# Kernel optimization log

Measured on AMD Instinct MI355X. Metric: run time of the kernel, lower is better.

Reference implementation:

```python
import jax, jax.numpy as jnp
import numpy as np

B, C, H, W = 2, 256, 32, 32
D_MODEL = C
D_INNER = 2 * D_MODEL          # 512
D_STATE = 16
DT_RANK = (D_MODEL + 15) // 16  # 16
D_CONV = 4
LN_EPS = 1e-5


def setup_inputs() -> dict:
    key = jax.random.key(0)
    ks = jax.random.split(key, 32)

    def nrm(k, shape, s=0.02):
        return (jax.random.normal(k, shape) * s).astype(jnp.float32)

    inp = {"x": jax.random.normal(ks[0], (B, C, H, W), dtype=jnp.float32)}
    # LayerNorm params
    inp["ln1_w"] = jnp.ones((D_MODEL,), jnp.float32)
    inp["ln1_b"] = jnp.zeros((D_MODEL,), jnp.float32)
    inp["ln2_w"] = jnp.ones((D_MODEL,), jnp.float32)
    inp["ln2_b"] = jnp.zeros((D_MODEL,), jnp.float32)
    # Two MambaBlocks with identical structure
    for i, p in enumerate(["m1", "m2"]):
        o = 1 + i * 11
        inp[p + "_in_w"] = nrm(ks[o + 0], (D_MODEL, 2 * D_INNER))
        inp[p + "_in_b"] = jnp.zeros((2 * D_INNER,), jnp.float32)
        inp[p + "_conv_w"] = nrm(ks[o + 1], (D_INNER, 1, D_CONV), 0.1)
        inp[p + "_conv_b"] = jnp.zeros((D_INNER,), jnp.float32)
        inp[p + "_xproj_w"] = nrm(ks[o + 2], (D_INNER, DT_RANK + 2 * D_STATE))
        inp[p + "_dt_w"] = nrm(ks[o + 3], (DT_RANK, D_INNER), 0.1)
        inp[p + "_dt_b"] = (jax.random.uniform(ks[o + 4], (D_INNER,)) * 0.1 - 4.0).astype(jnp.float32)
        # S4D-real init: A[d, n] = n+1
        inp[p + "_A_log"] = jnp.log(jnp.broadcast_to(jnp.arange(1, D_STATE + 1, dtype=jnp.float32), (D_INNER, D_STATE)))
        inp[p + "_D"] = jnp.ones((D_INNER,), jnp.float32)
        inp[p + "_out_w"] = nrm(ks[o + 5], (D_INNER, D_MODEL))
        inp[p + "_out_b"] = jnp.zeros((D_MODEL,), jnp.float32)
    return inp


def layernorm(x, w, b):
    mu = jnp.mean(x, axis=-1, keepdims=True)
    var = jnp.mean(jnp.square(x - mu), axis=-1, keepdims=True)
    return (x - mu) * jax.lax.rsqrt(var + LN_EPS) * w + b


def mamba_block(x, in_w, in_b, conv_w, conv_b, xproj_w, dt_w, dt_b, A_log, Dp, out_w, out_b):
    # x: (b, h, w, c) -> flatten spatial dims into the scan sequence
    b, h, w, c = x.shape
    L = h * w
    u = x.reshape(b, L, c)
    xr = u @ in_w + in_b                       # (b, L, 2*d_inner)
    xs, res = jnp.split(xr, 2, axis=-1)
    # depthwise causal conv1d over L
    xc = jnp.transpose(xs, (0, 2, 1))          # (b, d_inner, L)
    xc = jax.lax.conv_general_dilated(
        xc, conv_w, (1,), [(D_CONV - 1, 0)],
        dimension_numbers=("NCH", "OIH", "NCH"),
        feature_group_count=D_INNER) + conv_b[None, :, None]
    xs = jax.nn.silu(jnp.transpose(xc, (0, 2, 1)))  # (b, L, d_inner)
    # input-dependent SSM params
    x_dbl = xs @ xproj_w                       # (b, L, dt_rank + 2*n)
    dt, Bm, Cm = jnp.split(x_dbl, [DT_RANK, DT_RANK + D_STATE], axis=-1)
    delta = jax.nn.softplus(dt @ dt_w + dt_b)  # (b, L, d_inner)
    A = -jnp.exp(A_log)                        # (d_inner, n)
    dA = jnp.exp(delta[..., None] * A)                         # (b, L, d, n)
    dBu = delta[..., None] * Bm[:, :, None, :] * xs[..., None]  # (b, L, d, n)

    def step(hst, ins):
        dA_t, dBu_t, C_t = ins
        hst = dA_t * hst + dBu_t               # (b, d, n)
        y_t = jnp.einsum("bdn,bn->bd", hst, C_t)
        return hst, y_t

    h0 = jnp.zeros((b, D_INNER, D_STATE), dtype=xs.dtype)
    _, ys = jax.lax.scan(step, h0,
                         (jnp.swapaxes(dA, 0, 1), jnp.swapaxes(dBu, 0, 1), jnp.swapaxes(Cm, 0, 1)))
    y = jnp.swapaxes(ys, 0, 1) + xs * Dp       # (b, L, d_inner)
    y = y * jax.nn.silu(res)
    out = y @ out_w + out_b                    # (b, L, c)
    return out.reshape(b, h, w, c)


def reference(x, ln1_w, ln1_b, ln2_w, ln2_b,
              m1_in_w, m1_in_b, m1_conv_w, m1_conv_b, m1_xproj_w, m1_dt_w, m1_dt_b, m1_A_log, m1_D, m1_out_w, m1_out_b,
              m2_in_w, m2_in_b, m2_conv_w, m2_conv_b, m2_xproj_w, m2_dt_w, m2_dt_b, m2_A_log, m2_D, m2_out_w, m2_out_b):
    xt = jnp.transpose(x, (0, 2, 3, 1))  # b c h w -> b h w c
    xt = xt + layernorm(mamba_block(xt, m1_in_w, m1_in_b, m1_conv_w, m1_conv_b, m1_xproj_w,
                                    m1_dt_w, m1_dt_b, m1_A_log, m1_D, m1_out_w, m1_out_b), ln1_w, ln1_b)
    xt = jnp.flip(xt, axis=3)  # flip channel axis, as in the original
    xt = xt + layernorm(mamba_block(xt, m2_in_w, m2_in_b, m2_conv_w, m2_conv_b, m2_xproj_w,
                                    m2_dt_w, m2_dt_b, m2_A_log, m2_D, m2_out_w, m2_out_b), ln2_w, ln2_b)
    xt = jnp.flip(xt, axis=3)
    return jnp.transpose(xt, (0, 3, 1, 2))  # b h w c -> b c h w
```

## Files before the change

### kernel.cpp

```cpp
#include <hip/hip_runtime.h>
#include <hip/hip_bf16.h>
#include <math.h>

#define L 1024
#define NB 2
#define DM 256
#define DI 512
#define DS 16
#define NC 64
#define CL 16

typedef unsigned int u32;
typedef unsigned short u16;
typedef short s16x8 __attribute__((ext_vector_type(8)));
typedef float f32x4 __attribute__((ext_vector_type(4)));

__device__ __forceinline__ float sigmoidf_(float x){ return 1.f/(1.f+__expf(-x)); }
__device__ __forceinline__ u16 f2bf(float v){
  u32 x = __float_as_uint(v);
  return (u16)((x + 0x7fffu + ((x >> 16) & 1u)) >> 16);
}
__device__ __forceinline__ float bf2f(u16 v){ return __uint_as_float((u32)v << 16); }

__device__ __forceinline__ void gload_lds16(const void* g, void* l){
  __builtin_amdgcn_global_load_lds((const __attribute__((address_space(1))) u32*)g,
                                   (__attribute__((address_space(3))) u32*)l, 16, 0, 0);
}

__device__ __forceinline__ void wave_reduce2(float& a, float& b){
  #pragma unroll
  for (int m=32; m; m>>=1){ a += __shfl_xor(a, m, 64); b += __shfl_xor(b, m, 64); }
}

#define SEG1 262144
#define SEG2 294912
#define SEG3 131072
#define SEGP (SEG1+SEG2+SEG3)
__global__ __launch_bounds__(256) void k_prep_trans(const float* __restrict__ x,
    float* __restrict__ u, u16* __restrict__ ub,
    const float* __restrict__ inw1, const float* __restrict__ xpw1, const float* __restrict__ dtw1, const float* __restrict__ outw1,
    const float* __restrict__ inw2, const float* __restrict__ xpw2, const float* __restrict__ dtw2, const float* __restrict__ outw2,
    u16* __restrict__ Wt1i, u16* __restrict__ Wt1x, u16* __restrict__ Wt1o,
    u16* __restrict__ Wt2i, u16* __restrict__ Wt2x, u16* __restrict__ Wt2o){
  __shared__ float T[64][65];
  if (blockIdx.x < 128){
    int t = threadIdx.x;
    int bidx = blockIdx.x;
    int lt = bidx & 15, ct = (bidx >> 4) & 3, b = bidx >> 6;
    int l0 = lt*64, c0 = ct*64;
    int lsub = (t & 15)*4, csub = t >> 4;
    #pragma unroll
    for (int i=0;i<4;++i){
      int c = csub + i*16;
      float4 v = *(const float4*)(x + ((size_t)(b*256 + c0 + c))*1024 + l0 + lsub);
      T[lsub+0][c]=v.x; T[lsub+1][c]=v.y; T[lsub+2][c]=v.z; T[lsub+3][c]=v.w;
    }
    __syncthreads();
    int cw = (t & 15)*4, lw = t >> 4;
    #pragma unroll
    for (int i=0;i<4;++i){
      int l = lw + i*16;
      float4 v = make_float4(T[l][cw], T[l][cw+1], T[l][cw+2], T[l][cw+3]);
      size_t o = ((size_t)(b*1024 + l0 + l))*256 + c0 + cw;
      *(float4*)(u + o) = v;
      *(ushort4*)(ub + o) = make_ushort4(f2bf(v.x), f2bf(v.y), f2bf(v.z), f2bf(v.w));
    }
    return;
  }
  int g = (blockIdx.x - 128)*256 + threadIdx.x;
  int p = g >= SEGP;
  int r = g - p*SEGP;
  const float* inw = p ? inw2 : inw1;  const float* xpw = p ? xpw2 : xpw1;
  const float* dtw = p ? dtw2 : dtw1;  const float* outw = p ? outw2 : outw1;
  u16* Wti = p ? Wt2i : Wt1i; u16* Wtx = p ? Wt2x : Wt1x;
  u16* Wto = p ? Wt2o : Wt1o;
  if (r < SEG1){
    int n = r >> 8, k = r & 255;
    Wti[r] = f2bf(inw[(size_t)k*1024 + n]);
  } else if (r < SEG1+SEG2){
    int q = r - SEG1; int n = q >> 9, k = q & 511;
    float v;
    if (n < 512){
      float acc = 0.f;
      #pragma unroll
      for (int j=0;j<16;++j) acc = fmaf(xpw[k*48 + j], dtw[j*512 + n], acc);
      v = acc;
    } else if (n < 544){
      v = xpw[k*48 + 16 + (n - 512)];
    } else v = 0.f;
    Wtx[q] = f2bf(v);
  } else {
    int q = r - SEG1 - SEG2; int n = q >> 9, k = q & 511;
    Wto[q] = f2bf(outw[(size_t)k*256 + n]);
  }
}

__global__ __launch_bounds__(256) void k_gemm_mfma(const u16* __restrict__ A,
    const u16* __restrict__ Wt, const float* __restrict__ bias,
    float* __restrict__ C, int M, int N, int K){
  __shared__ __align__(16) u16 As[64*64];
  __shared__ __align__(16) u16 Bs[64*64];
  int tid = threadIdx.x, lane = tid & 63, wid = tid >> 6;
  int bm = blockIdx.y * 64, bn = blockIdx.x * 64;
  int wm = (wid >> 1) * 32, wn = (wid & 1) * 32;
  int lrow = lane & 15, lg = lane >> 4;
  int srow = tid >> 3, ssl = tid & 7;
  int sswz = ssl ^ (srow & 7);
  f32x4 acc[2][2] = {};
  for (int k0 = 0; k0 < K; k0 += 64){
    #pragma unroll
    for (int i = 0; i < 2; ++i){
      int row = srow + i*32;
      gload_lds16(A  + (size_t)(bm + row)*K + k0 + sswz*8, &As[row*64 + ssl*8]);
      gload_lds16(Wt + (size_t)(bn + row)*K + k0 + sswz*8, &Bs[row*64 + ssl*8]);
    }
    __syncthreads();
    #pragma unroll
    for (int ks = 0; ks < 2; ++ks){
      int kg = ks*4 + lg;
      int swz = (kg ^ (lrow & 7)) << 3;
      s16x8 a[2], b[2];
      #pragma unroll
      for (int f = 0; f < 2; ++f){
        a[f] = *(const s16x8*)&As[(wm + f*16 + lrow)*64 + swz];
        b[f] = *(const s16x8*)&Bs[(wn + f*16 + lrow)*64 + swz];
      }
      #pragma unroll
      for (int i = 0; i < 2; ++i)
        #pragma unroll
        for (int j = 0; j < 2; ++j)
          acc[i][j] = __builtin_amdgcn_mfma_f32_16x16x32_bf16(a[i], b[j], acc[i][j], 0, 0, 0);
    }
    __syncthreads();
  }
  #pragma unroll
  for (int j = 0; j < 2; ++j){
    int col = bn + wn + j*16 + lrow;
    if (col < N){
      float bv = bias ? bias[col] : 0.f;
      #pragma unroll
      for (int i = 0; i < 2; ++i)
        #pragma unroll
        for (int r = 0; r < 4; ++r){
          int row = bm + wm + i*16 + lg*4 + r;
          C[(size_t)row*N + col] = acc[i][j][r] + bv;
        }
    }
  }
}

__global__ __launch_bounds__(256) void k_conv_t(const float* __restrict__ xr,
    const float* __restrict__ cw, const float* __restrict__ cb,
    u16* __restrict__ xscT, u16* __restrict__ xscbl, u16* __restrict__ sresT){
  __shared__ float T[67*68];
  int tid = threadIdx.x;
  int d0 = (blockIdx.x & 7) * 64;
  int bm = (blockIdx.x >> 3) * 64;
  bool bstart = (bm & 1023) == 0;
  for (int base = tid; base < 67*16; base += 256){
    int r = base >> 4, q = base & 15;
    float4 v;
    if (r < 3 && bstart) v = make_float4(0.f,0.f,0.f,0.f);
    else v = *(const float4*)(xr + (size_t)(bm - 3 + r)*1024 + d0 + q*4);
    *(float4*)&T[r*68 + q*4] = v;
  }
  __syncthreads();
  int d_local = tid >> 2, lseg = tid & 3;
  int d = d0 + d_local;
  float4 wv = *(const float4*)(cw + d*4);
  float cbv = cb[d];
  float fo[16];
  float xm3 = T[(lseg*16+0)*68 + d_local];
  float xm2 = T[(lseg*16+1)*68 + d_local];
  float xm1 = T[(lseg*16+2)*68 + d_local];
  #pragma unroll
  for (int i=0;i<16;++i){
    float xc = T[(lseg*16+i+3)*68 + d_local];
    float o = cbv;
    o = fmaf(wv.x, xm3, o); o = fmaf(wv.y, xm2, o);
    o = fmaf(wv.z, xm1, o); o = fmaf(wv.w, xc, o);
    o *= sigmoidf_(o);
    fo[i] = o;
    xm3 = xm2; xm2 = xm1; xm1 = xc;
  }
  {
    s16x8 v0, v1;
    #pragma unroll
    for (int i=0;i<8;++i){ v0[i] = (short)f2bf(fo[i]); v1[i] = (short)f2bf(fo[8+i]); }
    u16* dst = xscT + (size_t)d*2048 + bm + lseg*16;
    *(s16x8*)dst = v0; *(s16x8*)(dst+8) = v1;
  }
  __syncthreads();
  #pragma unroll
  for (int i=0;i<16;++i) T[(lseg*16+i+3)*68 + d_local] = fo[i];
  __syncthreads();
  {
    int l_local = tid >> 2, dseg = tid & 3;
    s16x8 p0, p1;
    #pragma unroll
    for (int i=0;i<8;++i){
      p0[i] = (short)f2bf(T[(l_local+3)*68 + dseg*16 + i]);
      p1[i] = (short)f2bf(T[(l_local+3)*68 + dseg*16 + 8 + i]);
    }
    u16* dst2 = xscbl + (size_t)(bm + l_local)*512 + d0 + dseg*16;
    *(s16x8*)dst2 = p0; *(s16x8*)(dst2+8) = p1;
  }
  __syncthreads();
  for (int base = tid; base < 64*16; base += 256){
    int r = base >> 4, q = base & 15;
    float4 v = *(const float4*)(xr + (size_t)(bm + r)*1024 + 512 + d0 + q*4);
    v.x *= sigmoidf_(v.x); v.y *= sigmoidf_(v.y);
    v.z *= sigmoidf_(v.z); v.w *= sigmoidf_(v.w);
    *(float4*)&T[r*68 + q*4] = v;
  }
  __syncthreads();
  {
    s16x8 r0, r1;
    #pragma unroll
    for (int i=0;i<8;++i){
      r0[i] = (short)f2bf(T[(lseg*16+i)*68 + d_local]);
      r1[i] = (short)f2bf(T[(lseg*16+8+i)*68 + d_local]);
    }
    u16* dst3 = sresT + (size_t)d*2048 + bm + lseg*16;
    *(s16x8*)dst3 = r0; *(s16x8*)(dst3+8) = r1;
  }
}

__global__ __launch_bounds__(256) void k_xproj(const u16* __restrict__ A,
    const u16* __restrict__ Wt, const float* __restrict__ dtb,
    u16* __restrict__ dltT, u16* __restrict__ BCb){
  __shared__ __align__(16) float smem[64*69];
  u16* As = (u16*)smem;
  u16* Bs = As + 4096;
  int tid = threadIdx.x, lane = tid & 63, wid = tid >> 6;
  int bn = blockIdx.x, bm = blockIdx.y * 64;
  int bn64 = bn * 64;
  int wm = (wid >> 1) * 32, wn = (wid & 1) * 32;
  int lrow = lane & 15, lg = lane >> 4;
  int srow = tid >> 3, ssl = tid & 7;
  int sswz = ssl ^ (srow & 7);
  f32x4 acc[2][2] = {};
  for (int k0 = 0; k0 < 512; k0 += 64){
    #pragma unroll
    for (int i = 0; i < 2; ++i){
      int row = srow + i*32;
      gload_lds16(A  + (size_t)(bm + row)*512 + k0 + sswz*8, &As[row*64 + ssl*8]);
      gload_lds16(Wt + (size_t)(bn64 + row)*512 + k0 + sswz*8, &Bs[row*64 + ssl*8]);
    }
    __syncthreads();
    #pragma unroll
    for (int ks = 0; ks < 2; ++ks){
      int kg = ks*4 + lg;
      int swz = (kg ^ (lrow & 7)) << 3;
      s16x8 a[2], b[2];
      #pragma unroll
      for (int f = 0; f < 2; ++f){
        a[f] = *(const s16x8*)&As[(wm + f*16 + lrow)*64 + swz];
        b[f] = *(const s16x8*)&Bs[(wn + f*16 + lrow)*64 + swz];
      }
      #pragma unroll
      for (int i = 0; i < 2; ++i)
        #pragma unroll
        for (int j = 0; j < 2; ++j)
          acc[i][j] = __builtin_amdgcn_mfma_f32_16x16x32_bf16(a[i], b[j], acc[i][j], 0, 0, 0);
    }
    __syncthreads();
  }
  if (bn < 8){
    float* DT = smem;
    #pragma unroll
    for (int j=0;j<2;++j){
      int col_l = wn + j*16 + lrow;
      float bv = dtb[bn64 + col_l];
      #pragma unroll
      for (int i=0;i<2;++i)
        #pragma unroll
        for (int r=0;r<4;++r){
          int row_l = wm + i*16 + lg*4 + r;
          float a = acc[i][j][r] + bv;
          DT[row_l*69 + col_l] = fmaxf(a, 0.f) + log1pf(__expf(-fabsf(a)));
        }
    }
    __syncthreads();
    int c_local = tid >> 2, lseg = tid & 3;
    int dcol = bn64 + c_local;
    s16x8 v0, v1;
    #pragma unroll
    for (int i=0;i<8;++i){
      v0[i] = (short)f2bf(DT[(lseg*16+i)*69 + c_local]);
      v1[i] = (short)f2bf(DT[(lseg*16+8+i)*69 + c_local]);
    }
    u16* dst = dltT + (size_t)dcol*2048 + bm + lseg*16;
    *(s16x8*)dst = v0; *(s16x8*)(dst+8) = v1;
  } else {
    #pragma unroll
    for (int j=0;j<2;++j){
      int col_g = bn64 + wn + j*16 + lrow;
      if (col_g < 544){
        #pragma unroll
        for (int i=0;i<2;++i)
          #pragma unroll
          for (int r=0;r<4;++r){
            int row = bm + wm + i*16 + lg*4 + r;
            BCb[(size_t)row*32 + (col_g - 512)] = f2bf(acc[i][j][r]);
          }
      }
    }
  }
}

__global__ __launch_bounds__(256) void k_scan(const u16* __restrict__ dltT,
    const u16* __restrict__ xscT, const u16* __restrict__ BCb,
    const u16* __restrict__ sresT, const float* __restrict__ A_log,
    const float* __restrict__ Dp, u16* __restrict__ ygb){
  __shared__ float hbuf[64][68];
  __shared__ float SsumL[64][4];
  int tid = threadIdx.x;
  int chunk = tid >> 2, dl = tid & 3;
  int b = blockIdx.x >> 7, d0 = (blockIdx.x & 127) << 2;
  int d = d0 + dl;
  float A[DS];
  #pragma unroll
  for (int n=0;n<DS;++n) A[n] = -__expf(A_log[d*DS + n]);
  size_t cbase = (size_t)d*2048 + b*1024 + chunk*16;
  s16x8 dv0 = *(const s16x8*)(dltT + cbase);
  s16x8 dv1 = *(const s16x8*)(dltT + cbase + 8);
  s16x8 xv0 = *(const s16x8*)(xscT + cbase);
  s16x8 xv1 = *(const s16x8*)(xscT + cbase + 8);
  float dr[16], xq[16];
  #pragma unroll
  for (int i=0;i<8;++i){
    dr[i] = bf2f((u16)dv0[i]); dr[8+i] = bf2f((u16)dv1[i]);
    xq[i] = bf2f((u16)xv0[i]); xq[8+i] = bf2f((u16)xv1[i]);
  }
  float h[DS];
  #pragma unroll
  for (int n=0;n<DS;++n) h[n] = 0.f;
  float S = 0.f;
  int rbase = b*1024 + chunk*16;
  #pragma unroll
  for (int t=0;t<16;++t){
    const u16* bp = BCb + (size_t)(rbase + t)*32;
    s16x8 b0 = *(const s16x8*)bp;
    s16x8 b1 = *(const s16x8*)(bp + 8);
    float dlt = dr[t]; S += dlt;
    float dx = dlt * xq[t];
    #pragma unroll
    for (int n=0;n<8;++n) h[n] = fmaf(__expf(dlt*A[n]), h[n], dx*bf2f((u16)b0[n]));
    #pragma unroll
    for (int n=0;n<8;++n) h[8+n] = fmaf(__expf(dlt*A[8+n]), h[8+n], dx*bf2f((u16)b1[n]));
  }
  #pragma unroll
  for (int n=0;n<DS;++n) hbuf[chunk][dl*16+n] = h[n];
  SsumL[chunk][dl] = S;
  __syncthreads();
  if (tid < 64){
    int dl2 = tid & 3, n2 = tid >> 2;
    float An = -__expf(A_log[(d0+dl2)*DS + n2]);
    float hh = 0.f;
    for (int c=0;c<NC;++c){
      float he  = hbuf[c][dl2*16+n2];
      float dec = __expf(An * SsumL[c][dl2]);
      float nh  = fmaf(dec, hh, he);
      hbuf[c][dl2*16+n2] = hh;
      hh = nh;
    }
  }
  __syncthreads();
  #pragma unroll
  for (int n=0;n<DS;++n) h[n] = hbuf[chunk][dl*16+n];
  s16x8 s0 = *(const s16x8*)(sresT + cbase);
  s16x8 s1 = *(const s16x8*)(sresT + cbase + 8);
  float sr[16];
  #pragma unroll
  for (int i=0;i<8;++i){ sr[i] = bf2f((u16)s0[i]); sr[8+i] = bf2f((u16)s1[i]); }
  float Dv = Dp[d];
  #pragma unroll
  for (int t=0;t<16;++t){
    const u16* bp = BCb + (size_t)(rbase + t)*32;
    s16x8 b0 = *(const s16x8*)bp;
    s16x8 b1 = *(const s16x8*)(bp + 8);
    s16x8 c0 = *(const s16x8*)(bp + 16);
    s16x8 c1 = *(const s16x8*)(bp + 24);
    float dlt = dr[t];
    float dx = dlt * xq[t];
    float y = 0.f;
    #pragma unroll
    for (int n=0;n<8;++n){
      h[n] = fmaf(__expf(dlt*A[n]), h[n], dx*bf2f((u16)b0[n]));
      y = fmaf(h[n], bf2f((u16)c0[n]), y);
    }
    #pragma unroll
    for (int n=0;n<8;++n){
      h[8+n] = fmaf(__expf(dlt*A[8+n]), h[8+n], dx*bf2f((u16)b1[n]));
      y = fmaf(h[8+n], bf2f((u16)c1[n]), y);
    }
    y = fmaf(xq[t], Dv, y);
    ygb[(size_t)(rbase + t)*512 + d] = f2bf(y * sr[t]);
  }
}

__global__ __launch_bounds__(256) void k_ln_flip(const float* __restrict__ mo, const float* __restrict__ resid,
    const float* __restrict__ w, const float* __restrict__ bias,
    float* __restrict__ u2, u16* __restrict__ u2b){
  int row = blockIdx.x*4 + (threadIdx.x >> 6);
  int lane = threadIdx.x & 63;
  int c4 = lane*4;
  float4 xv = *(const float4*)(mo + (size_t)row*256 + c4);
  float s1 = xv.x+xv.y+xv.z+xv.w;
  float s2 = xv.x*xv.x+xv.y*xv.y+xv.z*xv.z+xv.w*xv.w;
  wave_reduce2(s1, s2);
  float mu = s1*(1.f/256), var = s2*(1.f/256) - mu*mu;
  float inv = rsqrtf(var + 1e-5f);
  float4 rv = *(const float4*)(resid + (size_t)row*256 + c4);
  float4 wv = *(const float4*)(w + c4);
  float4 bv = *(const float4*)(bias + c4);
  float o0 = rv.x + (xv.x-mu)*inv*wv.x + bv.x;
  float o1 = rv.y + (xv.y-mu)*inv*wv.y + bv.y;
  float o2 = rv.z + (xv.z-mu)*inv*wv.z + bv.z;
  float o3 = rv.w + (xv.w-mu)*inv*wv.w + bv.w;
  size_t o = (size_t)row*256 + (252 - c4);
  *(float4*)(u2 + o) = make_float4(o3, o2, o1, o0);
  *(ushort4*)(u2b + o) = make_ushort4(f2bf(o3), f2bf(o2), f2bf(o1), f2bf(o0));
}

__global__ __launch_bounds__(256) void k_ln_out(const float* __restrict__ mo, const float* __restrict__ resid,
    const float* __restrict__ w, const float* __restrict__ bias, float* __restrict__ out){
  int row = blockIdx.x*4 + (threadIdx.x >> 6);
  int lane = threadIdx.x & 63;
  int c4 = lane*4;
  int b = row >> 10, l = row & 1023;
  float4 xv = *(const float4*)(mo + (size_t)row*256 + c4);
  float s1 = xv.x+xv.y+xv.z+xv.w;
  float s2 = xv.x*xv.x+xv.y*xv.y+xv.z*xv.z+xv.w*xv.w;
  wave_reduce2(s1, s2);
  float mu = s1*(1.f/256), var = s2*(1.f/256) - mu*mu;
  float inv = rsqrtf(var + 1e-5f);
  float4 rv = *(const float4*)(resid + (size_t)row*256 + c4);
  float4 wv = *(const float4*)(w + c4);
  float4 bv = *(const float4*)(bias + c4);
  float o0 = rv.x + (xv.x-mu)*inv*wv.x + bv.x;
  float o1 = rv.y + (xv.y-mu)*inv*wv.y + bv.y;
  float o2 = rv.z + (xv.z-mu)*inv*wv.z + bv.z;
  float o3 = rv.w + (xv.w-mu)*inv*wv.w + bv.w;
  size_t base = ((size_t)b*256 + 255) << 10;
  out[base - ((size_t)(c4+0) << 10) + l] = o0;
  out[base - ((size_t)(c4+1) << 10) + l] = o1;
  out[base - ((size_t)(c4+2) << 10) + l] = o2;
  out[base - ((size_t)(c4+3) << 10) + l] = o3;
}

extern "C" void kernel_launch(void* const* d_in, const int* in_sizes, int n_in,
                              void* d_out, int out_size, void* d_ws, size_t ws_size,
                              hipStream_t stream) {
  const float* x    = (const float*)d_in[0];
  const float* ln1w = (const float*)d_in[1];
  const float* ln1b = (const float*)d_in[2];
  const float* ln2w = (const float*)d_in[3];
  const float* ln2b = (const float*)d_in[4];

  const float* m1[11]; const float* m2[11];
  for (int i=0;i<11;++i){ m1[i] = (const float*)d_in[5+i]; m2[i] = (const float*)d_in[16+i]; }

  float* ws = (float*)d_ws;
  float* u0    = ws;
  u16*   u0b   = (u16*)(ws + 524288);
  float* xr    = ws + 655360;
  u16*   xscbl = (u16*)(ws + 2752512);
  u16*   xscT  = (u16*)(ws + 3276800);
  u16*   sresT = (u16*)(ws + 3801088);
  u16*   dltT  = (u16*)(ws + 4325376);
  u16*   BCb   = (u16*)(ws + 4849664);
  u16*   ygb   = (u16*)(ws + 4882432);
  float* mo    = ws + 5406720;
  float* u2    = ws + 5931008;
  u16*   u2b   = (u16*)(ws + 6455296);
  u16*   Wt1i  = (u16*)(ws + 6586368);
  u16*   Wt1x  = (u16*)(ws + 6717440);
  u16*   Wt1o  = (u16*)(ws + 6864896);
  u16*   Wt2i  = (u16*)(ws + 6930432);
  u16*   Wt2x  = (u16*)(ws + 7061504);
  u16*   Wt2o  = (u16*)(ws + 7208960);

  dim3 b256(256);
  k_prep_trans<<<128 + 2*SEGP/256, b256, 0, stream>>>(x, u0, u0b,
      m1[0], m1[4], m1[5], m1[9], m2[0], m2[4], m2[5], m2[9],
      Wt1i, Wt1x, Wt1o, Wt2i, Wt2x, Wt2o);

  k_gemm_mfma<<<dim3(16,32), b256, 0, stream>>>(u0b, Wt1i, m1[1], xr, NB*L, 2*DI, DM);
  k_conv_t<<<256, b256, 0, stream>>>(xr, m1[2], m1[3], xscT, xscbl, sresT);
  k_xproj<<<dim3(9,32), b256, 0, stream>>>(xscbl, Wt1x, m1[6], dltT, BCb);
  k_scan<<<256, b256, 0, stream>>>(dltT, xscT, BCb, sresT, m1[7], m1[8], ygb);
  k_gemm_mfma<<<dim3(4,32), b256, 0, stream>>>(ygb, Wt1o, m1[10], mo, NB*L, DM, DI);
  k_ln_flip<<<512, b256, 0, stream>>>(mo, u0, ln1w, ln1b, u2, u2b);

  k_gemm_mfma<<<dim3(16,32), b256, 0, stream>>>(u2b, Wt2i, m2[1], xr, NB*L, 2*DI, DM);
  k_conv_t<<<256, b256, 0, stream>>>(xr, m2[2], m2[3], xscT, xscbl, sresT);
  k_xproj<<<dim3(9,32), b256, 0, stream>>>(xscbl, Wt2x, m2[6], dltT, BCb);
  k_scan<<<256, b256, 0, stream>>>(dltT, xscT, BCb, sresT, m2[7], m2[8], ygb);
  k_gemm_mfma<<<dim3(4,32), b256, 0, stream>>>(ygb, Wt2o, m2[10], mo, NB*L, DM, DI);
  k_ln_out<<<512, b256, 0, stream>>>(mo, u2, ln2w, ln2b, (float*)d_out);
}
```

Measured before the change: 128.1 us.

## Fuse in-proj epilogue with silu/transpose and out-proj with layernorm

The in-projection GEMM now writes the xs half directly as bf16 and applies silu plus a transpose to the residual half in its epilogue. This removes the fp32 xr intermediate and the residual pass that lived in the conv kernel. The out-projection GEMM is fused with layernorm, the residual add and the flip/transpose writes by having each block own full 256-column rows, which eliminates the mo buffer and two LN kernels. The trade-off is that the out-proj launch drops to only 32 blocks, so GPU occupancy is low, and xs is now rounded to bf16 before the conv.

Measured after the change: 138.0 us. 7.8% more time.

```diff
diff --git a/kernel.cpp b/kernel.cpp
--- a/kernel.cpp
+++ b/kernel.cpp
@@ -25,11 +25,6 @@
 __device__ __forceinline__ void gload_lds16(const void* g, void* l){
   __builtin_amdgcn_global_load_lds((const __attribute__((address_space(1))) u32*)g,
                                    (__attribute__((address_space(3))) u32*)l, 16, 0, 0);
-}
-
-__device__ __forceinline__ void wave_reduce2(float& a, float& b){
-  #pragma unroll
-  for (int m=32; m; m>>=1){ a += __shfl_xor(a, m, 64); b += __shfl_xor(b, m, 64); }
 }
 
 #define SEG1 262144
@@ -95,24 +90,26 @@
   }
 }
 
-__global__ __launch_bounds__(256) void k_gemm_mfma(const u16* __restrict__ A,
+__global__ __launch_bounds__(256) void k_in_proj(const u16* __restrict__ A,
     const u16* __restrict__ Wt, const float* __restrict__ bias,
-    float* __restrict__ C, int M, int N, int K){
-  __shared__ __align__(16) u16 As[64*64];
-  __shared__ __align__(16) u16 Bs[64*64];
+    u16* __restrict__ xsb, u16* __restrict__ sresT){
+  __shared__ __align__(16) float smem[64*65];
+  u16* As = (u16*)smem;
+  u16* Bs = As + 4096;
   int tid = threadIdx.x, lane = tid & 63, wid = tid >> 6;
-  int bm = blockIdx.y * 64, bn = blockIdx.x * 64;
+  int bn = blockIdx.x, bm = blockIdx.y * 64;
+  int bn64 = bn * 64;
   int wm = (wid >> 1) * 32, wn = (wid & 1) * 32;
   int lrow = lane & 15, lg = lane >> 4;
   int srow = tid >> 3, ssl = tid & 7;
   int sswz = ssl ^ (srow & 7);
   f32x4 acc[2][2] = {};
-  for (int k0 = 0; k0 < K; k0 += 64){
+  for (int k0 = 0; k0 < 256; k0 += 64){
     #pragma unroll
     for (int i = 0; i < 2; ++i){
       int row = srow + i*32;
-      gload_lds16(A  + (size_t)(bm + row)*K + k0 + sswz*8, &As[row*64 + ssl*8]);
-      gload_lds16(Wt + (size_t)(bn + row)*K + k0 + sswz*8, &Bs[row*64 + ssl*8]);
+      gload_lds16(A  + (size_t)(bm + row)*256 + k0 + sswz*8, &As[row*64 + ssl*8]);
+      gload_lds16(Wt + (size_t)(bn64 + row)*256 + k0 + sswz*8, &Bs[row*64 + ssl*8]);
     }
     __syncthreads();
     #pragma unroll
@@ -133,36 +130,68 @@
     }
     __syncthreads();
   }
-  #pragma unroll
-  for (int j = 0; j < 2; ++j){
-    int col = bn + wn + j*16 + lrow;
-    if (col < N){
-      float bv = bias ? bias[col] : 0.f;
-      #pragma unroll
-      for (int i = 0; i < 2; ++i)
-        #pragma unroll
-        for (int r = 0; r < 4; ++r){
-          int row = bm + wm + i*16 + lg*4 + r;
-          C[(size_t)row*N + col] = acc[i][j][r] + bv;
+  if (bn < 8){
+    #pragma unroll
+    for (int j=0;j<2;++j){
+      int col_l = wn + j*16 + lrow;
+      float bv = bias[bn64 + col_l];
+      #pragma unroll
+      for (int i=0;i<2;++i)
+        #pragma unroll
+        for (int r=0;r<4;++r){
+          int row_l = wm + i*16 + lg*4 + r;
+          xsb[(size_t)(bm + row_l)*512 + bn64 + col_l] = f2bf(acc[i][j][r] + bv);
         }
     }
-  }
-}
-
-__global__ __launch_bounds__(256) void k_conv_t(const float* __restrict__ xr,
+  } else {
+    float* CT = smem;
+    #pragma unroll
+    for (int j=0;j<2;++j){
+      int col_l = wn + j*16 + lrow;
+      float bv = bias[bn64 + col_l];
+      #pragma unroll
+      for (int i=0;i<2;++i)
+        #pragma unroll
+        for (int r=0;r<4;++r){
+          int row_l = wm + i*16 + lg*4 + r;
+          float o = acc[i][j][r] + bv;
+          CT[row_l*65 + col_l] = o * sigmoidf_(o);
+        }
+    }
+    __syncthreads();
+    int d_local = tid >> 2, lseg = tid & 3;
+    s16x8 r0, r1;
+    #pragma unroll
+    for (int i=0;i<8;++i){
+      r0[i] = (short)f2bf(CT[(lseg*16+i)*65 + d_local]);
+      r1[i] = (short)f2bf(CT[(lseg*16+8+i)*65 + d_local]);
+    }
+    u16* dst = sresT + (size_t)(bn64 - 512 + d_local)*2048 + bm + lseg*16;
+    *(s16x8*)dst = r0; *(s16x8*)(dst+8) = r1;
+  }
+}
+
+__global__ __launch_bounds__(256) void k_conv_t(const u16* __restrict__ xsb,
     const float* __restrict__ cw, const float* __restrict__ cb,
-    u16* __restrict__ xscT, u16* __restrict__ xscbl, u16* __restrict__ sresT){
+    u16* __restrict__ xscT, u16* __restrict__ xscbl){
   __shared__ float T[67*68];
   int tid = threadIdx.x;
   int d0 = (blockIdx.x & 7) * 64;
   int bm = (blockIdx.x >> 3) * 64;
   bool bstart = (bm & 1023) == 0;
-  for (int base = tid; base < 67*16; base += 256){
-    int r = base >> 4, q = base & 15;
-    float4 v;
-    if (r < 3 && bstart) v = make_float4(0.f,0.f,0.f,0.f);
-    else v = *(const float4*)(xr + (size_t)(bm - 3 + r)*1024 + d0 + q*4);
-    *(float4*)&T[r*68 + q*4] = v;
+  for (int base = tid; base < 67*8; base += 256){
+    int r = base >> 3, q = base & 7;
+    float v[8];
+    if (r < 3 && bstart){
+      #pragma unroll
+      for (int k=0;k<8;++k) v[k] = 0.f;
+    } else {
+      s16x8 hv = *(const s16x8*)(xsb + (size_t)(bm - 3 + r)*512 + d0 + q*8);
+      #pragma unroll
+      for (int k=0;k<8;++k) v[k] = bf2f((u16)hv[k]);
+    }
+    #pragma unroll
+    for (int k=0;k<8;++k) T[r*68 + q*8 + k] = v[k];
   }
   __syncthreads();
   int d_local = tid >> 2, lseg = tid & 3;
@@ -204,25 +233,6 @@
     }
     u16* dst2 = xscbl + (size_t)(bm + l_local)*512 + d0 + dseg*16;
     *(s16x8*)dst2 = p0; *(s16x8*)(dst2+8) = p1;
-  }
-  __syncthreads();
-  for (int base = tid; base < 64*16; base += 256){
-    int r = base >> 4, q = base & 15;
-    float4 v = *(const float4*)(xr + (size_t)(bm + r)*1024 + 512 + d0 + q*4);
-    v.x *= sigmoidf_(v.x); v.y *= sigmoidf_(v.y);
-    v.z *= sigmoidf_(v.z); v.w *= sigmoidf_(v.w);
-    *(float4*)&T[r*68 + q*4] = v;
-  }
-  __syncthreads();
-  {
-    s16x8 r0, r1;
-    #pragma unroll
-    for (int i=0;i<8;++i){
-      r0[i] = (short)f2bf(T[(lseg*16+i)*68 + d_local]);
-      r1[i] = (short)f2bf(T[(lseg*16+8+i)*68 + d_local]);
-    }
-    u16* dst3 = sresT + (size_t)d*2048 + bm + lseg*16;
-    *(s16x8*)dst3 = r0; *(s16x8*)(dst3+8) = r1;
   }
 }
 
@@ -400,54 +410,93 @@
   }
 }
 
-__global__ __launch_bounds__(256) void k_ln_flip(const float* __restrict__ mo, const float* __restrict__ resid,
-    const float* __restrict__ w, const float* __restrict__ bias,
-    float* __restrict__ u2, u16* __restrict__ u2b){
-  int row = blockIdx.x*4 + (threadIdx.x >> 6);
-  int lane = threadIdx.x & 63;
-  int c4 = lane*4;
-  float4 xv = *(const float4*)(mo + (size_t)row*256 + c4);
-  float s1 = xv.x+xv.y+xv.z+xv.w;
-  float s2 = xv.x*xv.x+xv.y*xv.y+xv.z*xv.z+xv.w*xv.w;
-  wave_reduce2(s1, s2);
-  float mu = s1*(1.f/256), var = s2*(1.f/256) - mu*mu;
-  float inv = rsqrtf(var + 1e-5f);
-  float4 rv = *(const float4*)(resid + (size_t)row*256 + c4);
-  float4 wv = *(const float4*)(w + c4);
-  float4 bv = *(const float4*)(bias + c4);
-  float o0 = rv.x + (xv.x-mu)*inv*wv.x + bv.x;
-  float o1 = rv.y + (xv.y-mu)*inv*wv.y + bv.y;
-  float o2 = rv.z + (xv.z-mu)*inv*wv.z + bv.z;
-  float o3 = rv.w + (xv.w-mu)*inv*wv.w + bv.w;
-  size_t o = (size_t)row*256 + (252 - c4);
-  *(float4*)(u2 + o) = make_float4(o3, o2, o1, o0);
-  *(ushort4*)(u2b + o) = make_ushort4(f2bf(o3), f2bf(o2), f2bf(o1), f2bf(o0));
-}
-
-__global__ __launch_bounds__(256) void k_ln_out(const float* __restrict__ mo, const float* __restrict__ resid,
-    const float* __restrict__ w, const float* __restrict__ bias, float* __restrict__ out){
-  int row = blockIdx.x*4 + (threadIdx.x >> 6);
-  int lane = threadIdx.x & 63;
-  int c4 = lane*4;
-  int b = row >> 10, l = row & 1023;
-  float4 xv = *(const float4*)(mo + (size_t)row*256 + c4);
-  float s1 = xv.x+xv.y+xv.z+xv.w;
-  float s2 = xv.x*xv.x+xv.y*xv.y+xv.z*xv.z+xv.w*xv.w;
-  wave_reduce2(s1, s2);
-  float mu = s1*(1.f/256), var = s2*(1.f/256) - mu*mu;
-  float inv = rsqrtf(var + 1e-5f);
-  float4 rv = *(const float4*)(resid + (size_t)row*256 + c4);
-  float4 wv = *(const float4*)(w + c4);
-  float4 bv = *(const float4*)(bias + c4);
-  float o0 = rv.x + (xv.x-mu)*inv*wv.x + bv.x;
-  float o1 = rv.y + (xv.y-mu)*inv*wv.y + bv.y;
-  float o2 = rv.z + (xv.z-mu)*inv*wv.z + bv.z;
-  float o3 = rv.w + (xv.w-mu)*inv*wv.w + bv.w;
-  size_t base = ((size_t)b*256 + 255) << 10;
-  out[base - ((size_t)(c4+0) << 10) + l] = o0;
-  out[base - ((size_t)(c4+1) << 10) + l] = o1;
-  out[base - ((size_t)(c4+2) << 10) + l] = o2;
-  out[base - ((size_t)(c4+3) << 10) + l] = o3;
+template<int MODE>
+__global__ __launch_bounds__(256) void k_gemm_out_ln(const u16* __restrict__ A,
+    const u16* __restrict__ Wt, const float* __restrict__ ob,
+    const float* __restrict__ resid, const float* __restrict__ lnw, const float* __restrict__ lnb,
+    float* __restrict__ out, u16* __restrict__ outb){
+  __shared__ __align__(16) u16 As[64*64];
+  __shared__ __align__(16) u16 Bs[256*64];
+  __shared__ float redS[2][64], redQ[2][64];
+  int tid = threadIdx.x, lane = tid & 63, wid = tid >> 6;
+  int bm = blockIdx.x * 64;
+  int wm = (wid & 1)*32, wn = (wid >> 1)*128;
+  int lrow = lane & 15, lg = lane >> 4;
+  int srow = tid >> 3, ssl = tid & 7;
+  int sswz = ssl ^ (srow & 7);
+  f32x4 acc[2][8] = {};
+  for (int k0=0;k0<512;k0+=64){
+    #pragma unroll
+    for (int i=0;i<2;++i){
+      int row = srow + i*32;
+      gload_lds16(A + (size_t)(bm+row)*512 + k0 + sswz*8, &As[row*64 + ssl*8]);
+    }
+    #pragma unroll
+    for (int i=0;i<8;++i){
+      int row = srow + i*32;
+      gload_lds16(Wt + (size_t)row*512 + k0 + sswz*8, &Bs[row*64 + ssl*8]);
+    }
+    __syncthreads();
+    #pragma unroll
+    for (int ks=0;ks<2;++ks){
+      int kg = ks*4 + lg;
+      int swz = (kg ^ (lrow & 7)) << 3;
+      s16x8 a[2], bq[8];
+      #pragma unroll
+      for (int f=0;f<2;++f) a[f] = *(const s16x8*)&As[(wm + f*16 + lrow)*64 + swz];
+      #pragma unroll
+      for (int j=0;j<8;++j) bq[j] = *(const s16x8*)&Bs[(wn + j*16 + lrow)*64 + swz];
+      #pragma unroll
+      for (int f=0;f<2;++f)
+        #pragma unroll
+        for (int j=0;j<8;++j)
+          acc[f][j] = __builtin_amdgcn_mfma_f32_16x16x32_bf16(a[f], bq[j], acc[f][j], 0, 0, 0);
+    }
+    __syncthreads();
+  }
+  float bv[8], lw[8], lb[8];
+  #pragma unroll
+  for (int j=0;j<8;++j){
+    int col = wn + j*16 + lrow;
+    bv[j] = ob[col]; lw[j] = lnw[col]; lb[j] = lnb[col];
+  }
+  #pragma unroll
+  for (int i=0;i<2;++i)
+    #pragma unroll
+    for (int r=0;r<4;++r){
+      float s=0.f, q=0.f;
+      #pragma unroll
+      for (int j=0;j<8;++j){ float v = acc[i][j][r] + bv[j]; s += v; q = fmaf(v, v, q); }
+      #pragma unroll
+      for (int m=1;m<=8;m<<=1){ s += __shfl_xor(s, m, 64); q += __shfl_xor(q, m, 64); }
+      if (lrow == 0){ int row = wm + i*16 + lg*4 + r; redS[wn>>7][row] = s; redQ[wn>>7][row] = q; }
+    }
+  __syncthreads();
+  #pragma unroll
+  for (int i=0;i<2;++i)
+    #pragma unroll
+    for (int r=0;r<4;++r){
+      int row = wm + i*16 + lg*4 + r;
+      int grow = bm + row;
+      float S = redS[0][row] + redS[1][row];
+      float Q = redQ[0][row] + redQ[1][row];
+      float mu = S * (1.f/256.f);
+      float var = Q * (1.f/256.f) - mu*mu;
+      float inv = rsqrtf(var + 1e-5f);
+      #pragma unroll
+      for (int j=0;j<8;++j){
+        int col = wn + j*16 + lrow;
+        float v = acc[i][j][r] + bv[j];
+        float o = resid[(size_t)grow*256 + col] + (v - mu)*inv*lw[j] + lb[j];
+        if (MODE == 0){
+          out[(size_t)grow*256 + 255 - col]  = o;
+          outb[(size_t)grow*256 + 255 - col] = f2bf(o);
+        } else {
+          int bb = grow >> 10, ll = grow & 1023;
+          out[(((size_t)bb*256) + (255 - col))*1024 + ll] = o;
+        }
+      }
+    }
 }
 
 extern "C" void kernel_launch(void* const* d_in, const int* in_sizes, int n_in,
@@ -465,39 +514,36 @@
   float* ws = (float*)d_ws;
   float* u0    = ws;
   u16*   u0b   = (u16*)(ws + 524288);
-  float* xr    = ws + 655360;
-  u16*   xscbl = (u16*)(ws + 2752512);
-  u16*   xscT  = (u16*)(ws + 3276800);
-  u16*   sresT = (u16*)(ws + 3801088);
-  u16*   dltT  = (u16*)(ws + 4325376);
-  u16*   BCb   = (u16*)(ws + 4849664);
-  u16*   ygb   = (u16*)(ws + 4882432);
-  float* mo    = ws + 5406720;
-  float* u2    = ws + 5931008;
-  u16*   u2b   = (u16*)(ws + 6455296);
-  u16*   Wt1i  = (u16*)(ws + 6586368);
-  u16*   Wt1x  = (u16*)(ws + 6717440);
-  u16*   Wt1o  = (u16*)(ws + 6864896);
-  u16*   Wt2i  = (u16*)(ws + 6930432);
-  u16*   Wt2x  = (u16*)(ws + 7061504);
-  u16*   Wt2o  = (u16*)(ws + 7208960);
+  u16*   xsb   = (u16*)(ws + 655360);
+  u16*   xscbl = (u16*)(ws + 1179648);
+  u16*   xscT  = (u16*)(ws + 1703936);
+  u16*   sresT = (u16*)(ws + 2228224);
+  u16*   dltT  = (u16*)(ws + 2752512);
+  u16*   BCb   = (u16*)(ws + 3276800);
+  u16*   ygb   = (u16*)(ws + 3309568);
+  float* u2    = ws + 3833856;
+  u16*   u2b   = (u16*)(ws + 4358144);
+  u16*   Wt1i  = (u16*)(ws + 4489216);
+  u16*   Wt1x  = (u16*)(ws + 4620288);
+  u16*   Wt1o  = (u16*)(ws + 4767744);
+  u16*   Wt2i  = (u16*)(ws + 4833280);
+  u16*   Wt2x  = (u16*)(ws + 4964352);
+  u16*   Wt2o  = (u16*)(ws + 5111808);
 
   dim3 b256(256);
   k_prep_trans<<<128 + 2*SEGP/256, b256, 0, stream>>>(x, u0, u0b,
       m1[0], m1[4], m1[5], m1[9], m2[0], m2[4], m2[5], m2[9],
       Wt1i, Wt1x, Wt1o, Wt2i, Wt2x, Wt2o);
 
-  k_gemm_mfma<<<dim3(16,32), b256, 0, stream>>>(u0b, Wt1i, m1[1], xr, NB*L, 2*DI, DM);
-  k_conv_t<<<256, b256, 0, stream>>>(xr, m1[2], m1[3], xscT, xscbl, sresT);
+  k_in_proj<<<dim3(16,32), b256, 0, stream>>>(u0b, Wt1i, m1[1], xsb, sresT);
+  k_conv_t<<<256, b256, 0, stream>>>(xsb, m1[2], m1[3], xscT, xscbl);
   k_xproj<<<dim3(9,32), b256, 0, stream>>>(xscbl, Wt1x, m1[6], dltT, BCb);
   k_scan<<<256, b256, 0, stream>>>(dltT, xscT, BCb, sresT, m1[7], m1[8], ygb);
-  k_gemm_mfma<<<dim3(4,32), b256, 0, stream>>>(ygb, Wt1o, m1[10], mo, NB*L, DM, DI);
-  k_ln_flip<<<512, b256, 0, stream>>>(mo, u0, ln1w, ln1b, u2, u2b);
-
-  k_gemm_mfma<<<dim3(16,32), b256, 0, stream>>>(u2b, Wt2i, m2[1], xr, NB*L, 2*DI, DM);
-  k_conv_t<<<256, b256, 0, stream>>>(xr, m2[2], m2[3], xscT, xscbl, sresT);
+  k_gemm_out_ln<0><<<32, b256, 0, stream>>>(ygb, Wt1o, m1[10], u0, ln1w, ln1b, u2, u2b);
+
+  k_in_proj<<<dim3(16,32), b256, 0, stream>>>(u2b, Wt2i, m2[1], xsb, sresT);
+  k_conv_t<<<256, b256, 0, stream>>>(xsb, m2[2], m2[3], xscT, xscbl);
   k_xproj<<<dim3(9,32), b256, 0, stream>>>(xscbl, Wt2x, m2[6], dltT, BCb);
   k_scan<<<256, b256, 0, stream>>>(dltT, xscT, BCb, sresT, m2[7], m2[8], ygb);
-  k_gemm_mfma<<<dim3(4,32), b256, 0, stream>>>(ygb, Wt2o, m2[10], mo, NB*L, DM, DI);
-  k_ln_out<<<512, b256, 0, stream>>>(mo, u2, ln2w, ln2b, (float*)d_out);
-}
+  k_gemm_out_ln<1><<<32, b256, 0, stream>>>(ygb, Wt2o, m2[10], u2, ln2w, ln2b, (float*)d_out, nullptr);
+}
```

## Fuse output projection GEMM with LayerNorm, residual, flip and transpose

Applied to the files above, without the earlier changes.

Replaces the separate out-projection GEMM plus LayerNorm kernels with one templated kernel. Each block computes a 16-row by 256-column tile with MFMA, reduces row statistics in LDS, and applies bias, LayerNorm, residual and the channel flip or output transpose in the epilogue. This removes the fp32 intermediate round trip through global memory and two kernel launches per block. In exchange the fused GEMM launches only 128 blocks that each loop over the full K, which may lower parallelism compared with the earlier tiled GEMM.

Measured after the change: 125.4 us (median of 3 runs). 1.02x faster.

```diff
diff --git a/kernel.cpp b/kernel.cpp
--- a/kernel.cpp
+++ b/kernel.cpp
@@ -25,11 +25,6 @@
 __device__ __forceinline__ void gload_lds16(const void* g, void* l){
   __builtin_amdgcn_global_load_lds((const __attribute__((address_space(1))) u32*)g,
                                    (__attribute__((address_space(3))) u32*)l, 16, 0, 0);
-}
-
-__device__ __forceinline__ void wave_reduce2(float& a, float& b){
-  #pragma unroll
-  for (int m=32; m; m>>=1){ a += __shfl_xor(a, m, 64); b += __shfl_xor(b, m, 64); }
 }
 
 #define SEG1 262144
@@ -400,54 +395,99 @@
   }
 }
 
-__global__ __launch_bounds__(256) void k_ln_flip(const float* __restrict__ mo, const float* __restrict__ resid,
-    const float* __restrict__ w, const float* __restrict__ bias,
-    float* __restrict__ u2, u16* __restrict__ u2b){
-  int row = blockIdx.x*4 + (threadIdx.x >> 6);
-  int lane = threadIdx.x & 63;
-  int c4 = lane*4;
-  float4 xv = *(const float4*)(mo + (size_t)row*256 + c4);
-  float s1 = xv.x+xv.y+xv.z+xv.w;
-  float s2 = xv.x*xv.x+xv.y*xv.y+xv.z*xv.z+xv.w*xv.w;
-  wave_reduce2(s1, s2);
-  float mu = s1*(1.f/256), var = s2*(1.f/256) - mu*mu;
-  float inv = rsqrtf(var + 1e-5f);
-  float4 rv = *(const float4*)(resid + (size_t)row*256 + c4);
-  float4 wv = *(const float4*)(w + c4);
-  float4 bv = *(const float4*)(bias + c4);
-  float o0 = rv.x + (xv.x-mu)*inv*wv.x + bv.x;
-  float o1 = rv.y + (xv.y-mu)*inv*wv.y + bv.y;
-  float o2 = rv.z + (xv.z-mu)*inv*wv.z + bv.z;
-  float o3 = rv.w + (xv.w-mu)*inv*wv.w + bv.w;
-  size_t o = (size_t)row*256 + (252 - c4);
-  *(float4*)(u2 + o) = make_float4(o3, o2, o1, o0);
-  *(ushort4*)(u2b + o) = make_ushort4(f2bf(o3), f2bf(o2), f2bf(o1), f2bf(o0));
-}
-
-__global__ __launch_bounds__(256) void k_ln_out(const float* __restrict__ mo, const float* __restrict__ resid,
-    const float* __restrict__ w, const float* __restrict__ bias, float* __restrict__ out){
-  int row = blockIdx.x*4 + (threadIdx.x >> 6);
-  int lane = threadIdx.x & 63;
-  int c4 = lane*4;
-  int b = row >> 10, l = row & 1023;
-  float4 xv = *(const float4*)(mo + (size_t)row*256 + c4);
-  float s1 = xv.x+xv.y+xv.z+xv.w;
-  float s2 = xv.x*xv.x+xv.y*xv.y+xv.z*xv.z+xv.w*xv.w;
-  wave_reduce2(s1, s2);
-  float mu = s1*(1.f/256), var = s2*(1.f/256) - mu*mu;
-  float inv = rsqrtf(var + 1e-5f);
-  float4 rv = *(const float4*)(resid + (size_t)row*256 + c4);
-  float4 wv = *(const float4*)(w + c4);
-  float4 bv = *(const float4*)(bias + c4);
-  float o0 = rv.x + (xv.x-mu)*inv*wv.x + bv.x;
-  float o1 = rv.y + (xv.y-mu)*inv*wv.y + bv.y;
-  float o2 = rv.z + (xv.z-mu)*inv*wv.z + bv.z;
-  float o3 = rv.w + (xv.w-mu)*inv*wv.w + bv.w;
-  size_t base = ((size_t)b*256 + 255) << 10;
-  out[base - ((size_t)(c4+0) << 10) + l] = o0;
-  out[base - ((size_t)(c4+1) << 10) + l] = o1;
-  out[base - ((size_t)(c4+2) << 10) + l] = o2;
-  out[base - ((size_t)(c4+3) << 10) + l] = o3;
+template<int MODE>
+__global__ __launch_bounds__(256) void k_out_ln(const u16* __restrict__ A,
+    const u16* __restrict__ Wt, const float* __restrict__ ob,
+    const float* __restrict__ resid, const float* __restrict__ lnw, const float* __restrict__ lnb,
+    float* __restrict__ out, u16* __restrict__ outb){
+  __shared__ __align__(16) u16 As[16*512];
+  __shared__ __align__(16) u16 Bs[256*64];
+  __shared__ float redS[4][16], redQ[4][16];
+  int tid = threadIdx.x, lane = tid & 63, wid = tid >> 6;
+  int bm = blockIdx.x * 16;
+  int wn = wid * 64;
+  int lrow = lane & 15, lg = lane >> 4;
+  #pragma unroll
+  for (int rd = 0; rd < 4; ++rd){
+    int e = rd*2048 + tid*8;
+    int r = e >> 9;
+    int s = (e >> 3) & 63;
+    gload_lds16(A + (size_t)(bm + r)*512 + ((s ^ (r & 7)) << 3), &As[e]);
+  }
+  int srow = tid >> 3, ssl = tid & 7;
+  f32x4 acc[4] = {};
+  for (int k0 = 0; k0 < 512; k0 += 64){
+    #pragma unroll
+    for (int i = 0; i < 8; ++i){
+      int row = srow + i*32;
+      gload_lds16(Wt + (size_t)row*512 + k0 + ((ssl ^ (row & 7)) << 3), &Bs[row*64 + ssl*8]);
+    }
+    __syncthreads();
+    #pragma unroll
+    for (int ks = 0; ks < 2; ++ks){
+      int kgl = ks*4 + lg;
+      int Sg = (k0 >> 3) + kgl;
+      s16x8 a = *(const s16x8*)&As[lrow*512 + ((Sg ^ (lrow & 7)) << 3)];
+      int swzb = (kgl ^ (lrow & 7)) << 3;
+      #pragma unroll
+      for (int j = 0; j < 4; ++j){
+        s16x8 b = *(const s16x8*)&Bs[(wn + j*16 + lrow)*64 + swzb];
+        acc[j] = __builtin_amdgcn_mfma_f32_16x16x32_bf16(a, b, acc[j], 0, 0, 0);
+      }
+    }
+    __syncthreads();
+  }
+  float bv[4], lwv[4], lbv[4];
+  #pragma unroll
+  for (int j=0;j<4;++j){
+    int col = wn + j*16 + lrow;
+    bv[j] = ob[col]; lwv[j] = lnw[col]; lbv[j] = lnb[col];
+  }
+  #pragma unroll
+  for (int r=0;r<4;++r){
+    float s=0.f, q=0.f;
+    #pragma unroll
+    for (int j=0;j<4;++j){ float v = acc[j][r] + bv[j]; s += v; q = fmaf(v,v,q); }
+    #pragma unroll
+    for (int m=1;m<=8;m<<=1){ s += __shfl_xor(s,m,64); q += __shfl_xor(q,m,64); }
+    if (lrow == 0){ redS[wid][lg*4+r] = s; redQ[wid][lg*4+r] = q; }
+  }
+  __syncthreads();
+  float* TT = (float*)Bs;
+  #pragma unroll
+  for (int r=0;r<4;++r){
+    int row_l = lg*4 + r;
+    int grow = bm + row_l;
+    float S = redS[0][row_l]+redS[1][row_l]+redS[2][row_l]+redS[3][row_l];
+    float Q = redQ[0][row_l]+redQ[1][row_l]+redQ[2][row_l]+redQ[3][row_l];
+    float mu = S*(1.f/256.f);
+    float var = Q*(1.f/256.f) - mu*mu;
+    float inv = rsqrtf(var + 1e-5f);
+    #pragma unroll
+    for (int j=0;j<4;++j){
+      int col = wn + j*16 + lrow;
+      float v = acc[j][r] + bv[j];
+      float o = resid[(size_t)grow*256 + col] + (v-mu)*inv*lwv[j] + lbv[j];
+      if (MODE == 0){
+        out[(size_t)grow*256 + 255 - col]  = o;
+        outb[(size_t)grow*256 + 255 - col] = f2bf(o);
+      } else {
+        TT[col*17 + row_l] = o;
+      }
+    }
+  }
+  if (MODE == 1){
+    __syncthreads();
+    int c = tid;
+    int b = bm >> 10, l0 = bm & 1023;
+    float vv[16];
+    #pragma unroll
+    for (int i=0;i<16;++i) vv[i] = TT[c*17 + i];
+    float* dst = out + ((size_t)(b*256) + (255 - c))*1024 + l0;
+    #pragma unroll
+    for (int i=0;i<4;++i)
+      *(float4*)(dst + i*4) = make_float4(vv[i*4], vv[i*4+1], vv[i*4+2], vv[i*4+3]);
+  }
 }
 
 extern "C" void kernel_launch(void* const* d_in, const int* in_sizes, int n_in,
@@ -472,15 +512,14 @@
   u16*   dltT  = (u16*)(ws + 4325376);
   u16*   BCb   = (u16*)(ws + 4849664);
   u16*   ygb   = (u16*)(ws + 4882432);
-  float* mo    = ws + 5406720;
-  float* u2    = ws + 5931008;
-  u16*   u2b   = (u16*)(ws + 6455296);
-  u16*   Wt1i  = (u16*)(ws + 6586368);
-  u16*   Wt1x  = (u16*)(ws + 6717440);
-  u16*   Wt1o  = (u16*)(ws + 6864896);
-  u16*   Wt2i  = (u16*)(ws + 6930432);
-  u16*   Wt2x  = (u16*)(ws + 7061504);
-  u16*   Wt2o  = (u16*)(ws + 7208960);
+  float* u2    = ws + 5406720;
+  u16*   u2b   = (u16*)(ws + 5931008);
+  u16*   Wt1i  = (u16*)(ws + 6062080);
+  u16*   Wt1x  = (u16*)(ws + 6193152);
+  u16*   Wt1o  = (u16*)(ws + 6340608);
+  u16*   Wt2i  = (u16*)(ws + 6406144);
+  u16*   Wt2x  = (u16*)(ws + 6537216);
+  u16*   Wt2o  = (u16*)(ws + 6684672);
 
   dim3 b256(256);
   k_prep_trans<<<128 + 2*SEGP/256, b256, 0, stream>>>(x, u0, u0b,
@@ -491,13 +530,11 @@
   k_conv_t<<<256, b256, 0, stream>>>(xr, m1[2], m1[3], xscT, xscbl, sresT);
   k_xproj<<<dim3(9,32), b256, 0, stream>>>(xscbl, Wt1x, m1[6], dltT, BCb);
   k_scan<<<256, b256, 0, stream>>>(dltT, xscT, BCb, sresT, m1[7], m1[8], ygb);
-  k_gemm_mfma<<<dim3(4,32), b256, 0, stream>>>(ygb, Wt1o, m1[10], mo, NB*L, DM, DI);
-  k_ln_flip<<<512, b256, 0, stream>>>(mo, u0, ln1w, ln1b, u2, u2b);
+  k_out_ln<0><<<128, b256, 0, stream>>>(ygb, Wt1o, m1[10], u0, ln1w, ln1b, u2, u2b);
 
   k_gemm_mfma<<<dim3(16,32), b256, 0, stream>>>(u2b, Wt2i, m2[1], xr, NB*L, 2*DI, DM);
   k_conv_t<<<256, b256, 0, stream>>>(xr, m2[2], m2[3], xscT, xscbl, sresT);
   k_xproj<<<dim3(9,32), b256, 0, stream>>>(xscbl, Wt2x, m2[6], dltT, BCb);
   k_scan<<<256, b256, 0, stream>>>(dltT, xscT, BCb, sresT, m2[7], m2[8], ygb);
-  k_gemm_mfma<<<dim3(4,32), b256, 0, stream>>>(ygb, Wt2o, m2[10], mo, NB*L, DM, DI);
-  k_ln_out<<<512, b256, 0, stream>>>(mo, u2, ln2w, ln2b, (float*)d_out);
-}
+  k_out_ln<1><<<128, b256, 0, stream>>>(ygb, Wt2o, m2[10], u2, ln2w, ln2b, (float*)d_out, nullptr);
+}
```
